# Kernel optimization log

Measured on AMD Instinct MI355X. Metric: run time of the kernel, lower is better.

## Reference

```python
import jax, jax.numpy as jnp
import numpy as np

HIDDEN = 2560
NUM_HEADS = 32
HEAD_DIM = HIDDEN // NUM_HEADS          # 80
ROTARY_DIM = int(0.4 * HEAD_DIM)        # 32 (partial rotary)
ROPE_BASE = 10000.0
SCALE = HEAD_DIM ** -0.5


def _apply_partial_rope(x, pos):
    # x: [B, S, H, D], pos: [B, S] int. NeoX-style rotation on first ROTARY_DIM dims.
    half = ROTARY_DIM // 2
    inv_freq = 1.0 / (ROPE_BASE ** (jnp.arange(half, dtype=jnp.float32) / half))
    ang = pos.astype(jnp.float32)[..., None] * inv_freq      # [B, S, half]
    cos = jnp.cos(ang)[:, :, None, :]                        # [B, S, 1, half]
    sin = jnp.sin(ang)[:, :, None, :]
    x1 = x[..., :half]
    x2 = x[..., half:ROTARY_DIM]
    x_pass = x[..., ROTARY_DIM:]
    o1 = x1 * cos - x2 * sin
    o2 = x2 * cos + x1 * sin
    return jnp.concatenate([o1, o2, x_pass], axis=-1)


def setup_inputs() -> dict:
    key = jax.random.key(0)
    ks = jax.random.split(key, 5)
    B, S = 2, 2048
    hidden_states = jax.random.normal(ks[0], (B, S, HIDDEN), dtype=jnp.float32)
    position_ids = jnp.tile(jnp.arange(S, dtype=jnp.int32)[None, :], (B, 1))
    w_std = HIDDEN ** -0.5
    Wqkv = jax.random.normal(ks[1], (HIDDEN, 3 * HIDDEN), dtype=jnp.float32) * w_std
    bqkv = jax.random.normal(ks[2], (3 * HIDDEN,), dtype=jnp.float32) * 0.02
    Wd = jax.random.normal(ks[3], (HIDDEN, HIDDEN), dtype=jnp.float32) * w_std
    bd = jax.random.normal(ks[4], (HIDDEN,), dtype=jnp.float32) * 0.02
    return {"position_ids": position_ids, "hidden_states": hidden_states,
            "Wqkv": Wqkv, "bqkv": bqkv, "Wd": Wd, "bd": bd}


def reference(position_ids, hidden_states, Wqkv, bqkv, Wd, bd):
    B, S, _ = hidden_states.shape
    qkv = hidden_states @ Wqkv + bqkv                         # [B, S, 3*HIDDEN]
    q, k, v = jnp.split(qkv, 3, axis=-1)
    q = q.reshape(B, S, NUM_HEADS, HEAD_DIM)
    k = k.reshape(B, S, NUM_HEADS, HEAD_DIM)
    v = v.reshape(B, S, NUM_HEADS, HEAD_DIM)
    q = _apply_partial_rope(q, position_ids)
    k = _apply_partial_rope(k, position_ids)
    # causal self-attention (RadixAttention prefill with empty prefix)
    scores = jnp.einsum('bqhd,bkhd->bhqk', q, k) * SCALE      # [B, H, S, S]
    causal = jnp.tril(jnp.ones((S, S), dtype=bool))
    scores = jnp.where(causal[None, None], scores, jnp.finfo(scores.dtype).min)
    probs = jax.nn.softmax(scores, axis=-1)
    attn = jnp.einsum('bhqk,bkhd->bqhd', probs, v).reshape(B, S, HIDDEN)
    return attn @ Wd + bd
```

## Files before the change

kernel.cpp:

```cpp
#include <hip/hip_runtime.h>

#define HIDDEN 2560
#define NHEADS 32
#define HDIM 80
#define DPAD 96
#define SEQ 2048
#define M_TOK 4096
#define N_QKV 7680
#define ATT_SCALE 0.11180339887498949f

typedef __attribute__((ext_vector_type(4))) float f32x4;
typedef __attribute__((ext_vector_type(16))) float f32x16;
typedef __attribute__((ext_vector_type(4))) int i32x4;
typedef __attribute__((ext_vector_type(8))) short bf16x8;
typedef __attribute__((ext_vector_type(8))) unsigned short ushort8;

#define BAR() asm volatile("s_barrier" ::: "memory")

__device__ __forceinline__ unsigned short f2bf(float f) {
    unsigned int u = __float_as_uint(f);
    u += 0x7FFFu + ((u >> 16) & 1u);
    return (unsigned short)(u >> 16);
}
__device__ __forceinline__ float bf2f(unsigned short h) {
    return __uint_as_float(((unsigned int)h) << 16);
}

__device__ __forceinline__ void async_copy16(unsigned short* lds, const unsigned short* g) {
    __builtin_amdgcn_global_load_lds((const __attribute__((address_space(1))) void*)g,
                                     (__attribute__((address_space(3))) void*)lds, 16, 0, 0);
}

__device__ __forceinline__ int cvt_pk_bf16(float lo, float hi) {
    int d;
    asm("v_cvt_pk_bf16_f32 %0, %1, %2" : "=v"(d) : "v"(lo), "v"(hi));
    return d;
}

__global__ __launch_bounds__(256) void cvt_kernel(const float* __restrict__ in,
                                                  unsigned short* __restrict__ out, int n8) {
    int i = blockIdx.x * 256 + threadIdx.x;
    if (i >= n8) return;
    const float4* p = (const float4*)in + (size_t)i * 2;
    float4 a = p[0], b = p[1];
    ushort8 o;
    o[0] = f2bf(a.x); o[1] = f2bf(a.y); o[2] = f2bf(a.z); o[3] = f2bf(a.w);
    o[4] = f2bf(b.x); o[5] = f2bf(b.y); o[6] = f2bf(b.z); o[7] = f2bf(b.w);
    *((ushort8*)out + i) = o;
}

__global__ __launch_bounds__(256) void transpose_kernel(const float* __restrict__ in,
                                                        unsigned short* __restrict__ out,
                                                        int R, int C) {
    __shared__ unsigned short tile[64][66];
    const int r0 = blockIdx.y * 64, c0 = blockIdx.x * 64;
    const int t = threadIdx.x;
#pragma unroll
    for (int rep = 0; rep < 16; ++rep) {
        int idx = rep * 256 + t;
        int i = idx >> 6, j = idx & 63;
        tile[i][j] = f2bf(in[(size_t)(r0 + i) * C + (c0 + j)]);
    }
    __syncthreads();
#pragma unroll
    for (int rep = 0; rep < 16; ++rep) {
        int idx = rep * 256 + t;
        int j = idx >> 6, i = idx & 63;
        out[(size_t)(c0 + j) * R + (r0 + i)] = tile[i][j];
    }
}

template <int OUT_BF16>
__global__ __launch_bounds__(512, 2) void gemm256(const unsigned short* __restrict__ A,
                                                  const unsigned short* __restrict__ Bt,
                                                  const float* __restrict__ bias,
                                                  void* __restrict__ C,
                                                  int M, int N, int K) {
    __shared__ __align__(16) unsigned short Alds[2][256 * 64];
    __shared__ __align__(16) unsigned short Blds[2][256 * 64];
    const int t = threadIdx.x;
    const int lane = t & 63, wid = t >> 6;
    const int wm = wid >> 2, wn = wid & 3;
    const int l15 = lane & 15, lhi = lane >> 4;

    const int cpx = (int)gridDim.x >> 3;
    const int wg = ((int)blockIdx.x % 8) * cpx + ((int)blockIdx.x >> 3);
    const int bm = (wg & 15) * 256;
    const int bn = (wg >> 4) * 256;

    int srow[4], scol[4];
#pragma unroll
    for (int c = 0; c < 4; ++c) {
        int idx = t + c * 512;
        srow[c] = idx >> 3;
        scol[c] = ((idx & 7) ^ (srow[c] & 7)) * 8;
    }
    const unsigned short* Abase = A + (size_t)bm * K;
    const unsigned short* Bbase = Bt + (size_t)bn * K;
    const int NT = K >> 6;

    auto stage = [&](int kt, int b) {
        const int k0 = kt << 6;
#pragma unroll
        for (int c = 0; c < 4; ++c)
            async_copy16(Alds[b] + (t + c * 512) * 8,
                         Abase + (size_t)srow[c] * K + k0 + scol[c]);
#pragma unroll
        for (int c = 0; c < 4; ++c)
            async_copy16(Blds[b] + (t + c * 512) * 8,
                         Bbase + (size_t)srow[c] * K + k0 + scol[c]);
    };

    f32x4 acc[8][4] = {};
    const int arow = wm * 128 + l15;
    const int brow = wn * 64 + l15;
    const int r7 = l15 & 7;

    stage(0, 0);
    stage(1, 1);

    for (int T = 0; T < NT; ++T) {
        const int b = T & 1;
        if (T < NT - 1) asm volatile("s_waitcnt vmcnt(8)" ::: "memory");
        else            asm volatile("s_waitcnt vmcnt(0)" ::: "memory");
        BAR();
        bf16x8 bq[4][2];
#pragma unroll
        for (int j = 0; j < 4; ++j)
#pragma unroll
            for (int kk = 0; kk < 2; ++kk)
                bq[j][kk] = *(const bf16x8*)(Blds[b] + (brow + j * 16) * 64 +
                                             (((kk * 4 + lhi) ^ r7) * 8));
#pragma unroll
        for (int q = 0; q < 4; ++q) {
            bf16x8 af2[2][2];
#pragma unroll
            for (int ii = 0; ii < 2; ++ii)
#pragma unroll
                for (int kk = 0; kk < 2; ++kk)
                    af2[ii][kk] = *(const bf16x8*)(Alds[b] + (arow + (q * 2 + ii) * 16) * 64 +
                                                   (((kk * 4 + lhi) ^ r7) * 8));
            __builtin_amdgcn_s_setprio(1);
#pragma unroll
            for (int ii = 0; ii < 2; ++ii)
#pragma unroll
                for (int j = 0; j < 4; ++j)
#pragma unroll
                    for (int kk = 0; kk < 2; ++kk)
                        acc[q * 2 + ii][j] = __builtin_amdgcn_mfma_f32_16x16x32_bf16(
                            af2[ii][kk], bq[j][kk], acc[q * 2 + ii][j], 0, 0, 0);
            __builtin_amdgcn_s_setprio(0);
            BAR();
        }
        if (T + 2 < NT) stage(T + 2, b);
    }

#pragma unroll
    for (int j = 0; j < 4; ++j) {
        const int col = bn + wn * 64 + j * 16 + l15;
        const float bv = bias[col];
#pragma unroll
        for (int i = 0; i < 8; ++i) {
            const int row0 = bm + wm * 128 + i * 16 + lhi * 4;
#pragma unroll
            for (int r = 0; r < 4; ++r) {
                float v = acc[i][j][r] + bv;
                if (OUT_BF16)
                    ((unsigned short*)C)[(size_t)(row0 + r) * N + col] = f2bf(v);
                else
                    ((float*)C)[(size_t)(row0 + r) * N + col] = v;
            }
        }
    }
}

__global__ __launch_bounds__(256) void pack_rope_kernel(const unsigned short* __restrict__ qkv,
                                                        const int* __restrict__ pos_ids,
                                                        unsigned short* __restrict__ Qb,
                                                        unsigned short* __restrict__ Kb,
                                                        unsigned short* __restrict__ Vt) {
    int g = blockIdx.x * 256 + threadIdx.x;
    int s = g & (SEQ - 1);
    int bh = g >> 11;
    int b = bh >> 5;
    int h = bh & 31;
    int m = b * SEQ + s;
    const unsigned short* base = qkv + (size_t)m * N_QKV + h * HDIM;
    unsigned short* Qrow = Qb + ((size_t)bh * SEQ + s) * DPAD;
    unsigned short* Krow = Kb + ((size_t)bh * SEQ + s) * DPAD;
    unsigned short* Vcol = Vt + (size_t)bh * HDIM * SEQ + s;

    float pos = (float)pos_ids[m];
    float qv[32], kv[32];
#pragma unroll
    for (int c = 0; c < 4; ++c) {
        ushort8 qc = *(const ushort8*)(base + c * 8);
        ushort8 kc = *(const ushort8*)(base + HIDDEN + c * 8);
#pragma unroll
        for (int j = 0; j < 8; ++j) {
            qv[c * 8 + j] = bf2f(qc[j]);
            kv[c * 8 + j] = bf2f(kc[j]);
        }
    }
#pragma unroll
    for (int d = 0; d < 16; ++d) {
        float inv = __expf(-(float)d * 0.5756462732485115f);
        float ang = pos * inv;
        float sn, cs;
        __sincosf(ang, &sn, &cs);
        float qcs = cs * ATT_SCALE, qsn = sn * ATT_SCALE;
        float x1 = qv[d], x2 = qv[d + 16];
        qv[d] = x1 * qcs - x2 * qsn;
        qv[d + 16] = x2 * qcs + x1 * qsn;
        x1 = kv[d]; x2 = kv[d + 16];
        kv[d] = x1 * cs - x2 * sn;
        kv[d + 16] = x2 * cs + x1 * sn;
    }
#pragma unroll
    for (int c = 0; c < 4; ++c) {
        ushort8 qo, ko;
#pragma unroll
        for (int j = 0; j < 8; ++j) {
            qo[j] = f2bf(qv[c * 8 + j]);
            ko[j] = f2bf(kv[c * 8 + j]);
        }
        *(ushort8*)(Qrow + c * 8) = qo;
        *(ushort8*)(Krow + c * 8) = ko;
    }
#pragma unroll
    for (int c = 4; c < 10; ++c) {
        ushort8 qc = *(const ushort8*)(base + c * 8);
        ushort8 qo;
#pragma unroll
        for (int j = 0; j < 8; ++j) qo[j] = f2bf(bf2f(qc[j]) * ATT_SCALE);
        *(ushort8*)(Qrow + c * 8) = qo;
        *(ushort8*)(Krow + c * 8) = *(const ushort8*)(base + HIDDEN + c * 8);
    }
    ushort8 z = {0, 0, 0, 0, 0, 0, 0, 0};
    *(ushort8*)(Qrow + 80) = z;
    *(ushort8*)(Qrow + 88) = z;
    *(ushort8*)(Krow + 80) = z;
    *(ushort8*)(Krow + 88) = z;
#pragma unroll
    for (int d = 0; d < HDIM; ++d) Vcol[(size_t)d * SEQ] = base[2 * HIDDEN + d];
}

__global__ __launch_bounds__(512) void flash_kernel(const unsigned short* __restrict__ Qb,
                                                    const unsigned short* __restrict__ Kb,
                                                    const unsigned short* __restrict__ Vt,
                                                    unsigned short* __restrict__ attn) {
    __shared__ __align__(16) unsigned short Klds[64 * 128];
    __shared__ __align__(16) unsigned short Vlds[96 * 64];

    const int bh = blockIdx.x;
    const int qb = 7 - (int)blockIdx.y;
    const int q0b = qb * 256;
    const int nkt = 4 * qb + 4;
    const int t = threadIdx.x;
    const int lane = t & 63, wid = t >> 6;
    const int l31 = lane & 31, h = lane >> 5, l7 = lane & 7;
    const int q0w = q0b + wid * 32;
    const int swz = l7 << 3;

    const unsigned short* Kbase = Kb + (size_t)bh * SEQ * DPAD;
    const unsigned short* Vbase = Vt + (size_t)bh * HDIM * SEQ;

    bf16x8 qf[6];
    {
        const unsigned short* Qrow = Qb + ((size_t)bh * SEQ + q0w + l31) * DPAD + h * 8;
#pragma unroll
        for (int dc = 0; dc < 6; ++dc) qf[dc] = *(const bf16x8*)(Qrow + dc * 16);
    }

    ((int*)Vlds)[2560 + t] = 0;

    f32x16 acc0 = {}, acc1 = {}, acc2 = {};
    float mrow = -1e30f, lrow = 0.f;

    const int kidx1 = 512 + t;
    const int kr0 = t / 12, kc0 = t % 12;
    const int kr1 = kidx1 / 12, kc1 = kidx1 % 12;
    const int vr0 = t >> 3, vc0 = t & 7;
    const int vr1 = (512 + t) >> 3, vc1 = t & 7;
    const int kd0 = kr0 * 128 + ((kc0 * 8) ^ ((kr0 & 7) << 3));
    const int kd1 = kr1 * 128 + ((kc1 * 8) ^ ((kr1 & 7) << 3));
    const int vd0 = vr0 * 64 + ((vc0 * 8) ^ ((vr0 & 7) << 3));
    const int vd1 = vr1 * 64 + ((vc1 * 8) ^ ((vr1 & 7) << 3));

    ushort8 kreg0, kreg1, vreg0, vreg1;
    kreg0 = *(const ushort8*)(Kbase + (size_t)t * 8);
    if (t < 256) kreg1 = *(const ushort8*)(Kbase + (size_t)kidx1 * 8);
    vreg0 = *(const ushort8*)(Vbase + (size_t)vr0 * SEQ + vc0 * 8);
    if (t < 128) vreg1 = *(const ushort8*)(Vbase + (size_t)vr1 * SEQ + vc1 * 8);

    for (int kt = 0; kt < nkt; ++kt) {
        const int k0 = kt * 64;
        __syncthreads();
        *(ushort8*)(Klds + kd0) = kreg0;
        if (t < 256) *(ushort8*)(Klds + kd1) = kreg1;
        *(ushort8*)(Vlds + vd0) = vreg0;
        if (t < 128) *(ushort8*)(Vlds + vd1) = vreg1;
        __syncthreads();
        if (kt + 1 < nkt) {
            const int kn = k0 + 64;
            kreg0 = *(const ushort8*)(Kbase + (size_t)kn * DPAD + (size_t)t * 8);
            if (t < 256) kreg1 = *(const ushort8*)(Kbase + (size_t)kn * DPAD + (size_t)kidx1 * 8);
            vreg0 = *(const ushort8*)(Vbase + (size_t)vr0 * SEQ + kn + vc0 * 8);
            if (t < 128) vreg1 = *(const ushort8*)(Vbase + (size_t)vr1 * SEQ + kn + vc1 * 8);
        }
        if (k0 > q0w + 31) continue;

        f32x16 s0 = {}, s1 = {};
        __builtin_amdgcn_s_setprio(1);
#pragma unroll
        for (int dc = 0; dc < 6; ++dc) {
            const int co = (dc * 16 + h * 8) ^ swz;
            bf16x8 ka = *(const bf16x8*)(Klds + l31 * 128 + co);
            bf16x8 kb2 = *(const bf16x8*)(Klds + (32 + l31) * 128 + co);
            s0 = __builtin_amdgcn_mfma_f32_32x32x16_bf16(ka, qf[dc], s0, 0, 0, 0);
            s1 = __builtin_amdgcn_mfma_f32_32x32x16_bf16(kb2, qf[dc], s1, 0, 0, 0);
        }
        __builtin_amdgcn_s_setprio(0);

        const int qg = q0w + l31;
        if (k0 + 63 > q0w) {
#pragma unroll
            for (int r = 0; r < 16; ++r) {
                const int kg = k0 + (r & 3) + 8 * (r >> 2) + 4 * h;
                if (kg > qg) s0[r] = -2e30f;
                if (kg + 32 > qg) s1[r] = -2e30f;
            }
        }
        float pmax = s0[0];
#pragma unroll
        for (int r = 1; r < 16; ++r) pmax = fmaxf(pmax, s0[r]);
#pragma unroll
        for (int r = 0; r < 16; ++r) pmax = fmaxf(pmax, s1[r]);
        pmax = fmaxf(pmax, __shfl_xor(pmax, 32, 64));
        if (!__all(pmax <= mrow + 8.0f)) {
            float mnew = fmaxf(mrow, pmax);
            float scl = __expf(mrow - mnew);
            mrow = mnew;
            lrow *= scl;
#pragma unroll
            for (int r = 0; r < 16; ++r) {
                float sq = __shfl(scl, (r & 3) + 8 * (r >> 2) + 4 * h, 64);
                acc0[r] *= sq; acc1[r] *= sq; acc2[r] *= sq;
            }
        }
        float ps = 0.f;
#pragma unroll
        for (int r = 0; r < 16; ++r) { s0[r] = __expf(s0[r] - mrow); ps += s0[r]; }
#pragma unroll
        for (int r = 0; r < 16; ++r) { s1[r] = __expf(s1[r] - mrow); ps += s1[r]; }
        lrow += ps + __shfl_xor(ps, 32, 64);
        i32x4 af[2][2];
#pragma unroll
        for (int ks = 0; ks < 2; ++ks) {
            const f32x16& sv = ks ? s1 : s0;
            int pk0[2], pk1[2], pk2[2], pk3[2];
#pragma unroll
            for (int i = 0; i < 2; ++i) {
                pk0[i] = cvt_pk_bf16(sv[2 * i], sv[2 * i + 1]);
                pk1[i] = cvt_pk_bf16(sv[4 + 2 * i], sv[5 + 2 * i]);
                pk2[i] = cvt_pk_bf16(sv[8 + 2 * i], sv[9 + 2 * i]);
                pk3[i] = cvt_pk_bf16(sv[12 + 2 * i], sv[13 + 2 * i]);
            }
#pragma unroll
            for (int i = 0; i < 2; ++i) {
                const int o0 = __shfl_xor(pk0[i], 32, 64);
                const int o1 = __shfl_xor(pk1[i], 32, 64);
                af[ks][0][i]     = h ? o1     : pk0[i];
                af[ks][0][2 + i] = h ? pk1[i] : o0;
                const int o2 = __shfl_xor(pk2[i], 32, 64);
                const int o3 = __shfl_xor(pk3[i], 32, 64);
                af[ks][1][i]     = h ? o3     : pk2[i];
                af[ks][1][2 + i] = h ? pk3[i] : o2;
            }
        }
        __builtin_amdgcn_s_setprio(1);
#pragma unroll
        for (int ds = 0; ds < 3; ++ds) {
            f32x16& ac = ds == 0 ? acc0 : (ds == 1 ? acc1 : acc2);
            const int vrow = (ds * 32 + l31) * 64;
#pragma unroll
            for (int ks = 0; ks < 2; ++ks)
#pragma unroll
                for (int kh = 0; kh < 2; ++kh) {
                    bf16x8 vb = *(const bf16x8*)(Vlds + vrow + ((ks * 32 + kh * 16 + h * 8) ^ swz));
                    bf16x8 pa = __builtin_bit_cast(bf16x8, af[ks][kh]);
                    ac = __builtin_amdgcn_mfma_f32_32x32x16_bf16(pa, vb, ac, 0, 0, 0);
                }
        }
        __builtin_amdgcn_s_setprio(0);
    }

    const int hh = bh & 31, b = bh >> 5;
    const float linv = 1.0f / lrow;
#pragma unroll
    for (int r = 0; r < 16; ++r) {
        const int ql = (r & 3) + 8 * (r >> 2) + 4 * h;
        const float lv = __shfl(linv, ql, 64);
        const int row = b * SEQ + q0b + wid * 32 + ql;
        unsigned short* orow = attn + (size_t)row * HIDDEN + hh * HDIM;
        orow[l31] = f2bf(acc0[r] * lv);
        orow[32 + l31] = f2bf(acc1[r] * lv);
        if (l31 < 16) orow[64 + l31] = f2bf(acc2[r] * lv);
    }
}

extern "C" void kernel_launch(void* const* d_in, const int* in_sizes, int n_in,
                              void* d_out, int out_size, void* d_ws, size_t ws_size,
                              hipStream_t stream) {
    const int* pos = (const int*)d_in[0];
    const float* hid = (const float*)d_in[1];
    const float* Wqkv = (const float*)d_in[2];
    const float* bqkv = (const float*)d_in[3];
    const float* Wd = (const float*)d_in[4];
    const float* bd = (const float*)d_in[5];
    float* out = (float*)d_out;
    char* ws = (char*)d_ws;

    unsigned short* WqkvT = (unsigned short*)(ws);
    unsigned short* WdT   = (unsigned short*)(ws + 39321600);
    unsigned short* Xbf   = (unsigned short*)(ws + 52428800);
    unsigned short* qkv   = (unsigned short*)(ws + 73400320);
    unsigned short* Qbuf  = (unsigned short*)(ws + 136314880);
    unsigned short* Kbuf  = (unsigned short*)(ws + 161480704);
    unsigned short* Vt    = (unsigned short*)(ws + 186646528);
    unsigned short* attnb = Xbf;

    cvt_kernel<<<(M_TOK * HIDDEN / 8 + 255) / 256, 256, 0, stream>>>(hid, Xbf, M_TOK * HIDDEN / 8);
    transpose_kernel<<<dim3(N_QKV / 64, HIDDEN / 64), 256, 0, stream>>>(Wqkv, WqkvT, HIDDEN, N_QKV);
    transpose_kernel<<<dim3(HIDDEN / 64, HIDDEN / 64), 256, 0, stream>>>(Wd, WdT, HIDDEN, HIDDEN);
    gemm256<1><<<(M_TOK / 256) * (N_QKV / 256), 512, 0, stream>>>(Xbf, WqkvT, bqkv, qkv,
                                                                  M_TOK, N_QKV, HIDDEN);
    pack_rope_kernel<<<(64 * SEQ) / 256, 256, 0, stream>>>(qkv, pos, Qbuf, Kbuf, Vt);
    flash_kernel<<<dim3(64, 8), 512, 0, stream>>>(Qbuf, Kbuf, Vt, attnb);
    gemm256<0><<<(M_TOK / 256) * (HIDDEN / 256), 512, 0, stream>>>(attnb, WdT, bd, out,
                                                                   M_TOK, HIDDEN, HIDDEN);
}
```

Before: 454.7 us.

## Restructure GEMM into four-stage K=32 LDS ring with interleaved async loads

Replaces the double-buffered K=64 GEMM main loop with a four-slot LDS ring of K=32 slices, three slices in flight. The A and B copies for the next slices are issued between the two MFMA halves of each period. This uses one barrier per period instead of five per K=64 tile and changes the LDS swizzle to match 32-wide rows. The goal is better overlap of global-to-LDS copies with MFMA work and less barrier overhead. The trade-offs are more loop periods and a hand-tuned vmcnt tail that must exactly match the copy counts.

```diff
diff --git a/kernel.cpp b/kernel.cpp
--- a/kernel.cpp
+++ b/kernel.cpp
@@ -76,8 +76,7 @@
                                                   const float* __restrict__ bias,
                                                   void* __restrict__ C,
                                                   int M, int N, int K) {
-    __shared__ __align__(16) unsigned short Alds[2][256 * 64];
-    __shared__ __align__(16) unsigned short Blds[2][256 * 64];
+    __shared__ __align__(16) unsigned short S[4][16384];
     const int t = threadIdx.x;
     const int lane = t & 63, wid = t >> 6;
     const int wm = wid >> 2, wn = wid & 3;
@@ -88,83 +87,101 @@
     const int bm = (wg & 15) * 256;
     const int bn = (wg >> 4) * 256;
 
-    int srow[4], scol[4];
-#pragma unroll
-    for (int c = 0; c < 4; ++c) {
+    int srow[2], scol[2];
+#pragma unroll
+    for (int c = 0; c < 2; ++c) {
         int idx = t + c * 512;
-        srow[c] = idx >> 3;
-        scol[c] = ((idx & 7) ^ (srow[c] & 7)) * 8;
+        srow[c] = idx >> 2;
+        scol[c] = ((idx & 3) ^ ((srow[c] >> 1) & 3)) * 8;
     }
     const unsigned short* Abase = A + (size_t)bm * K;
     const unsigned short* Bbase = Bt + (size_t)bn * K;
     const int NT = K >> 6;
 
-    auto stage = [&](int kt, int b) {
-        const int k0 = kt << 6;
-#pragma unroll
-        for (int c = 0; c < 4; ++c)
-            async_copy16(Alds[b] + (t + c * 512) * 8,
-                         Abase + (size_t)srow[c] * K + k0 + scol[c]);
-#pragma unroll
-        for (int c = 0; c < 4; ++c)
-            async_copy16(Blds[b] + (t + c * 512) * 8,
-                         Bbase + (size_t)srow[c] * K + k0 + scol[c]);
-    };
+    int aoff[8], boff[4];
+#pragma unroll
+    for (int i = 0; i < 8; ++i) {
+        int r = wm * 128 + i * 16 + l15;
+        aoff[i] = r * 32 + ((lhi ^ ((r >> 1) & 3)) * 8);
+    }
+#pragma unroll
+    for (int f = 0; f < 4; ++f) {
+        int r = wn * 64 + f * 16 + l15;
+        boff[f] = 8192 + r * 32 + ((lhi ^ ((r >> 1) & 3)) * 8);
+    }
 
     f32x4 acc[8][4] = {};
-    const int arow = wm * 128 + l15;
-    const int brow = wn * 64 + l15;
-    const int r7 = l15 & 7;
-
-    stage(0, 0);
-    stage(1, 1);
-
-    for (int T = 0; T < NT; ++T) {
-        const int b = T & 1;
-        if (T < NT - 1) asm volatile("s_waitcnt vmcnt(8)" ::: "memory");
-        else            asm volatile("s_waitcnt vmcnt(0)" ::: "memory");
-        BAR();
-        bf16x8 bq[4][2];
-#pragma unroll
-        for (int j = 0; j < 4; ++j)
-#pragma unroll
-            for (int kk = 0; kk < 2; ++kk)
-                bq[j][kk] = *(const bf16x8*)(Blds[b] + (brow + j * 16) * 64 +
-                                             (((kk * 4 + lhi) ^ r7) * 8));
-#pragma unroll
-        for (int q = 0; q < 4; ++q) {
-            bf16x8 af2[2][2];
-#pragma unroll
-            for (int ii = 0; ii < 2; ++ii)
-#pragma unroll
-                for (int kk = 0; kk < 2; ++kk)
-                    af2[ii][kk] = *(const bf16x8*)(Alds[b] + (arow + (q * 2 + ii) * 16) * 64 +
-                                                   (((kk * 4 + lhi) ^ r7) * 8));
-            __builtin_amdgcn_s_setprio(1);
-#pragma unroll
-            for (int ii = 0; ii < 2; ++ii)
-#pragma unroll
-                for (int j = 0; j < 4; ++j)
-#pragma unroll
-                    for (int kk = 0; kk < 2; ++kk)
-                        acc[q * 2 + ii][j] = __builtin_amdgcn_mfma_f32_16x16x32_bf16(
-                            af2[ii][kk], bq[j][kk], acc[q * 2 + ii][j], 0, 0, 0);
-            __builtin_amdgcn_s_setprio(0);
-            BAR();
-        }
-        if (T + 2 < NT) stage(T + 2, b);
-    }
-
-#pragma unroll
-    for (int j = 0; j < 4; ++j) {
-        const int col = bn + wn * 64 + j * 16 + l15;
+
+#define STAGE_A(J) { const int j_ = (J); unsigned short* d = &S[j_ & 3][0];            \
+    _Pragma("unroll")                                                                  \
+    for (int c = 0; c < 2; ++c)                                                        \
+        async_copy16(d + (t + c * 512) * 8,                                            \
+                     Abase + (size_t)srow[c] * K + j_ * 32 + scol[c]); }
+#define STAGE_B(J) { const int j_ = (J); unsigned short* d = &S[j_ & 3][8192];         \
+    _Pragma("unroll")                                                                  \
+    for (int c = 0; c < 2; ++c)                                                        \
+        async_copy16(d + (t + c * 512) * 8,                                            \
+                     Bbase + (size_t)srow[c] * K + j_ * 32 + scol[c]); }
+
+#define PERIOD(J, VM, DOSTAGE) {                                                       \
+    const int jp_ = (J);                                                               \
+    asm volatile("s_waitcnt vmcnt(" #VM ")" ::: "memory");                             \
+    BAR();                                                                             \
+    const unsigned short* sl = &S[jp_ & 3][0];                                         \
+    if (DOSTAGE) STAGE_A(jp_ + 3);                                                     \
+    bf16x8 bq[4], afr[4];                                                              \
+    _Pragma("unroll")                                                                  \
+    for (int f = 0; f < 4; ++f) bq[f] = *(const bf16x8*)(sl + boff[f]);                \
+    _Pragma("unroll")                                                                  \
+    for (int i = 0; i < 4; ++i) afr[i] = *(const bf16x8*)(sl + aoff[i]);               \
+    __builtin_amdgcn_s_setprio(1);                                                     \
+    _Pragma("unroll")                                                                  \
+    for (int i = 0; i < 4; ++i)                                                        \
+        _Pragma("unroll")                                                              \
+        for (int f = 0; f < 4; ++f)                                                    \
+            acc[i][f] = __builtin_amdgcn_mfma_f32_16x16x32_bf16(afr[i], bq[f],         \
+                                                                acc[i][f], 0, 0, 0);   \
+    __builtin_amdgcn_s_setprio(0);                                                     \
+    if (DOSTAGE) STAGE_B(jp_ + 3);                                                     \
+    _Pragma("unroll")                                                                  \
+    for (int i = 0; i < 4; ++i) afr[i] = *(const bf16x8*)(sl + aoff[4 + i]);           \
+    __builtin_amdgcn_s_setprio(1);                                                     \
+    _Pragma("unroll")                                                                  \
+    for (int i = 0; i < 4; ++i)                                                        \
+        _Pragma("unroll")                                                              \
+        for (int f = 0; f < 4; ++f)                                                    \
+            acc[4 + i][f] = __builtin_amdgcn_mfma_f32_16x16x32_bf16(afr[i], bq[f],     \
+                                                                    acc[4 + i][f],     \
+                                                                    0, 0, 0);          \
+    __builtin_amdgcn_s_setprio(0); }
+
+    STAGE_A(0); STAGE_B(0);
+    STAGE_A(1); STAGE_B(1);
+    STAGE_A(2); STAGE_B(2);
+
+    for (int T = 0; T < NT - 2; ++T) {
+        PERIOD(2 * T, 8, 1);
+        PERIOD(2 * T + 1, 8, 1);
+    }
+    PERIOD(2 * NT - 4, 8, 1);
+    PERIOD(2 * NT - 3, 8, 0);
+    PERIOD(2 * NT - 2, 4, 0);
+    PERIOD(2 * NT - 1, 0, 0);
+
+#undef PERIOD
+#undef STAGE_A
+#undef STAGE_B
+
+#pragma unroll
+    for (int f = 0; f < 4; ++f) {
+        const int col = bn + wn * 64 + f * 16 + l15;
         const float bv = bias[col];
 #pragma unroll
         for (int i = 0; i < 8; ++i) {
             const int row0 = bm + wm * 128 + i * 16 + lhi * 4;
 #pragma unroll
             for (int r = 0; r < 4; ++r) {
-                float v = acc[i][j][r] + bv;
+                float v = acc[i][f][r] + bv;
                 if (OUT_BF16)
                     ((unsigned short*)C)[(size_t)(row0 + r) * N + col] = f2bf(v);
                 else
```

Result: faster. 388.2 us (-14.6%).
